# Optimization experiments

Hardware: AMD Instinct MI355X
Metric: run time of the kernel (lower is better)

Reference implementation:

```python
import jax, jax.numpy as jnp
import numpy as np

N, E, D, H = 50000, 800000, 128, 128
LN_EPS = 1e-3  # keras LayerNormalization default epsilon


def layer_norm(x, g, b):
    mu = jnp.mean(x, axis=-1, keepdims=True)
    var = jnp.mean(jnp.square(x - mu), axis=-1, keepdims=True)
    return (x - mu) * jax.lax.rsqrt(var + LN_EPS) * g + b


def mlp3(x, W1, b1, W2, b2, W3, b3, g1, be1, g2, be2):
    # 3-layer MLP: two hidden layers (relu + layernorm), linear output head
    h = layer_norm(jax.nn.relu(x @ W1 + b1), g1, be1)
    h = layer_norm(jax.nn.relu(h @ W2 + b2), g2, be2)
    return h @ W3 + b3


def _dense_init(key, fan_in, fan_out):
    return jax.random.normal(key, (fan_in, fan_out), jnp.float32) / np.sqrt(fan_in)


def setup_inputs() -> dict:
    key = jax.random.key(0)
    ks = jax.random.split(key, 12)
    query = jax.random.normal(ks[0], (N, D), jnp.float32)
    memory = jax.random.normal(ks[1], (N, D), jnp.float32)
    row = jnp.sort(jax.random.randint(ks[2], (E,), 0, N, jnp.int32))
    col = jax.random.randint(ks[3], (E,), 0, N, jnp.int32)
    # pre_process MLP: input 2D -> H -> H -> 1 (heads=1)
    pW1 = _dense_init(ks[4], 2 * D, H); pb1 = jnp.zeros((H,), jnp.float32)
    pW2 = _dense_init(ks[5], H, H);     pb2 = jnp.zeros((H,), jnp.float32)
    pW3 = _dense_init(ks[6], H, 1);     pb3 = jnp.zeros((1,), jnp.float32)
    pg1 = jnp.ones((H,), jnp.float32);  pbe1 = jnp.zeros((H,), jnp.float32)
    pg2 = jnp.ones((H,), jnp.float32);  pbe2 = jnp.zeros((H,), jnp.float32)
    # memory MLP: D -> H -> H -> H
    mW1 = _dense_init(ks[7], D, H); mb1 = jnp.zeros((H,), jnp.float32)
    mW2 = _dense_init(ks[8], H, H); mb2 = jnp.zeros((H,), jnp.float32)
    mW3 = _dense_init(ks[9], H, H); mb3 = jnp.zeros((H,), jnp.float32)
    mg1 = jnp.ones((H,), jnp.float32); mbe1 = jnp.zeros((H,), jnp.float32)
    mg2 = jnp.ones((H,), jnp.float32); mbe2 = jnp.zeros((H,), jnp.float32)
    return dict(query=query, memory=memory, row=row, col=col,
                pW1=pW1, pb1=pb1, pW2=pW2, pb2=pb2, pW3=pW3, pb3=pb3,
                pg1=pg1, pbe1=pbe1, pg2=pg2, pbe2=pbe2,
                mW1=mW1, mb1=mb1, mW2=mW2, mb2=mb2, mW3=mW3, mb3=mb3,
                mg1=mg1, mbe1=mbe1, mg2=mg2, mbe2=mbe2)


def reference(query, memory, row, col,
              pW1, pb1, pW2, pb2, pW3, pb3, pg1, pbe1, pg2, pbe2,
              mW1, mb1, mW2, mb2, mW3, mb3, mg1, mbe1, mg2, mbe2):
    # per-edge gather of query (target) and memory (source) node features
    units = jnp.concatenate([query[row], memory[col]], axis=-1)  # [E, 2D]
    h = jnp.tanh(mlp3(units, pW1, pb1, pW2, pb2, pW3, pb3, pg1, pbe1, pg2, pbe2))[:, 0]  # [E]
    mem_head = mlp3(memory, mW1, mb1, mW2, mb2, mW3, mb3, mg1, mbe1, mg2, mbe2)  # [N, H]
    # sparse_dense_matmul: out[i] = sum_{edges (i,j)} h_e * mem_head[j]
    out = jax.ops.segment_sum(h[:, None] * mem_head[col], row, num_segments=N)  # [N, H]
    return out
```

## Files before the change

### kernel.cpp

```cpp
#include <hip/hip_runtime.h>
#include <hip/hip_bf16.h>

typedef __attribute__((ext_vector_type(8))) short  svec8;
typedef __attribute__((ext_vector_type(4))) short  svec4;
typedef __attribute__((ext_vector_type(8))) __bf16 bfvec8;
typedef __attribute__((ext_vector_type(4))) float  f32x4;
typedef __attribute__((ext_vector_type(2))) float  f32x2;
typedef __attribute__((ext_vector_type(4))) unsigned uvec4;

#define LN_EPS 1e-3f

__device__ __forceinline__ short f2bf(float f) {
  union { float f; unsigned u; } v; v.f = f;
  unsigned u = v.u;
  u += 0x7fff + ((u >> 16) & 1);
  return (short)(u >> 16);
}

__device__ __forceinline__ unsigned pk2(float a, float b) {
  unsigned short ua = __builtin_bit_cast(unsigned short, (__bf16)a);
  unsigned short ub = __builtin_bit_cast(unsigned short, (__bf16)b);
  return (unsigned)ua | ((unsigned)ub << 16);
}

__device__ __forceinline__ f32x2 up2(unsigned w) {
  f32x2 r;
  r[0] = __builtin_bit_cast(float, w << 16);
  r[1] = __builtin_bit_cast(float, w & 0xffff0000u);
  return r;
}

__device__ __forceinline__ f32x4 mfma16(svec8 a, svec8 b, f32x4 c) {
  return __builtin_amdgcn_mfma_f32_16x16x32_bf16(
      __builtin_bit_cast(bfvec8, a), __builtin_bit_cast(bfvec8, b), c, 0, 0, 0);
}

__global__ __launch_bounds__(256) void setup_kernel(
    const float* __restrict__ pW1, const float* __restrict__ pW2,
    const float* __restrict__ pg1,
    const float* __restrict__ mW1, const float* __restrict__ mW2,
    const float* __restrict__ mW3,
    short* __restrict__ w1qp, short* __restrict__ w1mp,
    short* __restrict__ w2p,  short* __restrict__ mw1p,
    short* __restrict__ mw2p, short* __restrict__ mw3p,
    const int* __restrict__ row, int E, int N, int* __restrict__ off,
    const float* __restrict__ g1, const float* __restrict__ be1,
    const float* __restrict__ b2, const float* __restrict__ g2,
    const float* __restrict__ w3, const float* __restrict__ be2,
    const float* __restrict__ b3,
    float* __restrict__ s2, float* __restrict__ b2pv,
    float* __restrict__ gw, float* __restrict__ consts, int nboff)
{
  const int b = blockIdx.x;
  const int tid = threadIdx.x;
  if (b < 384) {
    int idx = b * 256 + tid;
    int which = idx >> 14, p = idx & 16383;
    int j = p & 7, lane = (p >> 3) & 63, t = p >> 9;
    int nf = t & 7, ks = t >> 3;
    int k = ks * 32 + (lane >> 4) * 8 + j;
    int n = nf * 16 + (lane & 15);
    const float* src; short* dst; float scale = 1.f;
    switch (which) {
      case 0:  src = pW1;         dst = w1qp; break;
      case 1:  src = pW1 + 16384; dst = w1mp; break;
      case 2:  src = pW2;         dst = w2p; scale = pg1[k]; break;
      case 3:  src = mW1;         dst = mw1p; break;
      case 4:  src = mW2;         dst = mw2p; break;
      default: src = mW3;         dst = mw3p; break;
    }
    dst[p] = f2bf(scale * src[k * 128 + n]);
  } else if (b < 384 + nboff) {
    int i = (b - 384) * 256 + tid;
    if (i > N) return;
    int lo = 0, hi = E;
    while (lo < hi) { int mid = (lo + hi) >> 1; if (row[mid] < i) lo = mid + 1; else hi = mid; }
    off[i] = lo;
  } else {
    __shared__ float tmp[256];
    int n = tid;
    if (n < 128) {
      float s = 0.f, bb = 0.f;
      for (int k = 0; k < 128; ++k) {
        float w = pW2[k * 128 + n];
        s  = fmaf(g1[k],  w, s);
        bb = fmaf(be1[k], w, bb);
      }
      s2[n]   = s;
      b2pv[n] = bb + b2[n];
      float g = g2[n] * w3[n];
      gw[n] = g;
      tmp[n]       = g;
      tmp[128 + n] = be2[n] * w3[n];
    }
    __syncthreads();
    if (n == 0) {
      float a = 0.f, c = 0.f;
      for (int i = 0; i < 128; ++i) { a += tmp[i]; c += tmp[128 + i]; }
      consts[0] = a;
      consts[1] = c + b3[0];
    }
  }
}

__global__ __launch_bounds__(256) void node_kernel(
    const float* __restrict__ mem, const float* __restrict__ query,
    const short* __restrict__ w1p, const short* __restrict__ w2p, const short* __restrict__ w3p,
    const short* __restrict__ wmp, const short* __restrict__ wqp,
    const float* __restrict__ b1v, const float* __restrict__ b2v, const float* __restrict__ b3v,
    const float* __restrict__ g1v, const float* __restrict__ be1v,
    const float* __restrict__ g2v, const float* __restrict__ be2v,
    const float* __restrict__ pb1,
    short* __restrict__ mhb, short* __restrict__ mwt, short* __restrict__ qwt,
    int N, int nbm)
{
  __shared__ short Xs[64 * 128];
  __shared__ short H1s[64 * 128];
  __shared__ float redA[4][64];
  __shared__ float redB[4][64];

  const int tid  = threadIdx.x;
  const int wv   = tid >> 6;
  const int lane = tid & 63;
  const int g16  = lane >> 4;
  const int l16  = lane & 15;
  const bool is_mem = (blockIdx.x < nbm);
  const int r0   = (is_mem ? blockIdx.x : blockIdx.x - nbm) * 64;
  const float* src = is_mem ? mem : query;

  #pragma unroll
  for (int it = 0; it < 8; ++it) {
    int c = tid + it * 256;
    int r = c >> 5;
    int part = c & 31;
    int gr = r0 + r; if (gr >= N) gr = N - 1;
    f32x4 v = *(const f32x4*)(src + (size_t)gr * 128 + part * 4);
    svec4 s;
    s[0] = f2bf(v[0]); s[1] = f2bf(v[1]); s[2] = f2bf(v[2]); s[3] = f2bf(v[3]);
    int b = (r * 256 + part * 8) ^ ((r & 7) << 4);
    *(svec4*)((char*)Xs + b) = s;
  }
  __syncthreads();

  const int nfb = wv * 2;
  const int col0 = wv * 32 + l16, col1 = col0 + 16;

  if (!is_mem) {
    f32x4 acc[4][2];
    #pragma unroll
    for (int mf = 0; mf < 4; ++mf) { f32x4 z = {0.f,0.f,0.f,0.f}; acc[mf][0] = z; acc[mf][1] = z; }
    #pragma unroll
    for (int ks = 0; ks < 4; ++ks) {
      svec8 bw0 = *(const svec8*)(wqp + (((ks * 8 + nfb + 0) * 64 + lane) << 3));
      svec8 bw1 = *(const svec8*)(wqp + (((ks * 8 + nfb + 1) * 64 + lane) << 3));
      #pragma unroll
      for (int mf = 0; mf < 4; ++mf) {
        int row = mf * 16 + l16;
        int byt = (row * 256 + ks * 64 + g16 * 16) ^ ((row & 7) << 4);
        svec8 a = *(const svec8*)((const char*)Xs + byt);
        acc[mf][0] = mfma16(a, bw0, acc[mf][0]);
        acc[mf][1] = mfma16(a, bw1, acc[mf][1]);
      }
    }
    float bi0 = pb1[col0], bi1 = pb1[col1];
    #pragma unroll
    for (int mf = 0; mf < 4; ++mf)
      #pragma unroll
      for (int r = 0; r < 4; ++r) {
        int rr = mf * 16 + g16 * 4 + r;
        int gr = r0 + rr;
        if (gr < N) {
          qwt[(size_t)gr * 128 + col0] = f2bf(acc[mf][0][r] + bi0);
          qwt[(size_t)gr * 128 + col1] = f2bf(acc[mf][1][r] + bi1);
        }
      }
    return;
  }

  f32x4 acc[4][2], accm[4][2];
  #pragma unroll
  for (int mf = 0; mf < 4; ++mf) {
    f32x4 z = {0.f,0.f,0.f,0.f};
    acc[mf][0] = z; acc[mf][1] = z; accm[mf][0] = z; accm[mf][1] = z;
  }
  #pragma unroll
  for (int ks = 0; ks < 4; ++ks) {
    svec8 bw0 = *(const svec8*)(w1p + (((ks * 8 + nfb + 0) * 64 + lane) << 3));
    svec8 bw1 = *(const svec8*)(w1p + (((ks * 8 + nfb + 1) * 64 + lane) << 3));
    svec8 bm0 = *(const svec8*)(wmp + (((ks * 8 + nfb + 0) * 64 + lane) << 3));
    svec8 bm1 = *(const svec8*)(wmp + (((ks * 8 + nfb + 1) * 64 + lane) << 3));
    #pragma unroll
    for (int mf = 0; mf < 4; ++mf) {
      int row = mf * 16 + l16;
      int byt = (row * 256 + ks * 64 + g16 * 16) ^ ((row & 7) << 4);
      svec8 a = *(const svec8*)((const char*)Xs + byt);
      acc[mf][0]  = mfma16(a, bw0, acc[mf][0]);
      acc[mf][1]  = mfma16(a, bw1, acc[mf][1]);
      accm[mf][0] = mfma16(a, bm0, accm[mf][0]);
      accm[mf][1] = mfma16(a, bm1, accm[mf][1]);
    }
  }
  #pragma unroll
  for (int mf = 0; mf < 4; ++mf)
    #pragma unroll
    for (int r = 0; r < 4; ++r) {
      int rr = mf * 16 + g16 * 4 + r;
      int gr = r0 + rr;
      if (gr < N) {
        mwt[(size_t)gr * 128 + col0] = f2bf(accm[mf][0][r]);
        mwt[(size_t)gr * 128 + col1] = f2bf(accm[mf][1][r]);
      }
    }

  float bi0 = b1v[col0], bi1 = b1v[col1];
  float ga0 = g1v[col0], ga1 = g1v[col1];
  float bb0 = be1v[col0], bb1 = be1v[col1];
  float y[4][2][4], ps[4][4], pq[4][4];
  #pragma unroll
  for (int mf = 0; mf < 4; ++mf)
    #pragma unroll
    for (int r = 0; r < 4; ++r) {
      float y0 = fmaxf(acc[mf][0][r] + bi0, 0.f);
      float y1 = fmaxf(acc[mf][1][r] + bi1, 0.f);
      y[mf][0][r] = y0; y[mf][1][r] = y1;
      ps[mf][r] = y0 + y1;
      pq[mf][r] = y0 * y0 + y1 * y1;
    }
  #pragma unroll
  for (int mk = 1; mk <= 8; mk <<= 1)
    #pragma unroll
    for (int mf = 0; mf < 4; ++mf)
      #pragma unroll
      for (int r = 0; r < 4; ++r) {
        ps[mf][r] += __shfl_xor(ps[mf][r], mk, 64);
        pq[mf][r] += __shfl_xor(pq[mf][r], mk, 64);
      }
  if (l16 == 0) {
    #pragma unroll
    for (int mf = 0; mf < 4; ++mf)
      #pragma unroll
      for (int r = 0; r < 4; ++r) {
        redA[wv][mf * 16 + g16 * 4 + r] = ps[mf][r];
        redB[wv][mf * 16 + g16 * 4 + r] = pq[mf][r];
      }
  }
  __syncthreads();
  #pragma unroll
  for (int mf = 0; mf < 4; ++mf)
    #pragma unroll
    for (int r = 0; r < 4; ++r) {
      int rr = mf * 16 + g16 * 4 + r;
      float s = redA[0][rr] + redA[1][rr] + redA[2][rr] + redA[3][rr];
      float q = redB[0][rr] + redB[1][rr] + redB[2][rr] + redB[3][rr];
      float mu = s * (1.f / 128.f);
      float var = fmaxf(q * (1.f / 128.f) - mu * mu, 0.f);
      float rstd = rsqrtf(var + LN_EPS);
      float z0 = (y[mf][0][r] - mu) * rstd * ga0 + bb0;
      float z1 = (y[mf][1][r] - mu) * rstd * ga1 + bb1;
      int by0 = (rr * 256 + col0 * 2) ^ ((rr & 7) << 4);
      int by1 = (rr * 256 + col1 * 2) ^ ((rr & 7) << 4);
      *(short*)((char*)H1s + by0) = f2bf(z0);
      *(short*)((char*)H1s + by1) = f2bf(z1);
    }
  __syncthreads();

  f32x4 acc2[4][2];
  #pragma unroll
  for (int mf = 0; mf < 4; ++mf) { f32x4 z = {0.f,0.f,0.f,0.f}; acc2[mf][0] = z; acc2[mf][1] = z; }
  #pragma unroll
  for (int ks = 0; ks < 4; ++ks) {
    svec8 bw0 = *(const svec8*)(w2p + (((ks * 8 + nfb + 0) * 64 + lane) << 3));
    svec8 bw1 = *(const svec8*)(w2p + (((ks * 8 + nfb + 1) * 64 + lane) << 3));
    #pragma unroll
    for (int mf = 0; mf < 4; ++mf) {
      int row = mf * 16 + l16;
      int byt = (row * 256 + ks * 64 + g16 * 16) ^ ((row & 7) << 4);
      svec8 a = *(const svec8*)((const char*)H1s + byt);
      acc2[mf][0] = mfma16(a, bw0, acc2[mf][0]);
      acc2[mf][1] = mfma16(a, bw1, acc2[mf][1]);
    }
  }

  float bi20 = b2v[col0], bi21 = b2v[col1];
  float ga20 = g2v[col0], ga21 = g2v[col1];
  float bb20 = be2v[col0], bb21 = be2v[col1];
  float y2[4][2][4];
  #pragma unroll
  for (int mf = 0; mf < 4; ++mf)
    #pragma unroll
    for (int r = 0; r < 4; ++r) {
      float y0 = fmaxf(acc2[mf][0][r] + bi20, 0.f);
      float y1 = fmaxf(acc2[mf][1][r] + bi21, 0.f);
      y2[mf][0][r] = y0; y2[mf][1][r] = y1;
      ps[mf][r] = y0 + y1;
      pq[mf][r] = y0 * y0 + y1 * y1;
    }
  #pragma unroll
  for (int mk = 1; mk <= 8; mk <<= 1)
    #pragma unroll
    for (int mf = 0; mf < 4; ++mf)
      #pragma unroll
      for (int r = 0; r < 4; ++r) {
        ps[mf][r] += __shfl_xor(ps[mf][r], mk, 64);
        pq[mf][r] += __shfl_xor(pq[mf][r], mk, 64);
      }
  if (l16 == 0) {
    #pragma unroll
    for (int mf = 0; mf < 4; ++mf)
      #pragma unroll
      for (int r = 0; r < 4; ++r) {
        redA[wv][mf * 16 + g16 * 4 + r] = ps[mf][r];
        redB[wv][mf * 16 + g16 * 4 + r] = pq[mf][r];
      }
  }
  __syncthreads();
  #pragma unroll
  for (int mf = 0; mf < 4; ++mf)
    #pragma unroll
    for (int r = 0; r < 4; ++r) {
      int rr = mf * 16 + g16 * 4 + r;
      float s = redA[0][rr] + redA[1][rr] + redA[2][rr] + redA[3][rr];
      float q = redB[0][rr] + redB[1][rr] + redB[2][rr] + redB[3][rr];
      float mu = s * (1.f / 128.f);
      float var = fmaxf(q * (1.f / 128.f) - mu * mu, 0.f);
      float rstd = rsqrtf(var + LN_EPS);
      float z0 = (y2[mf][0][r] - mu) * rstd * ga20 + bb20;
      float z1 = (y2[mf][1][r] - mu) * rstd * ga21 + bb21;
      int by0 = (rr * 256 + col0 * 2) ^ ((rr & 7) << 4);
      int by1 = (rr * 256 + col1 * 2) ^ ((rr & 7) << 4);
      *(short*)((char*)Xs + by0) = f2bf(z0);
      *(short*)((char*)Xs + by1) = f2bf(z1);
    }
  __syncthreads();

  f32x4 acc3[4][2];
  #pragma unroll
  for (int mf = 0; mf < 4; ++mf) { f32x4 z = {0.f,0.f,0.f,0.f}; acc3[mf][0] = z; acc3[mf][1] = z; }
  #pragma unroll
  for (int ks = 0; ks < 4; ++ks) {
    svec8 bw0 = *(const svec8*)(w3p + (((ks * 8 + nfb + 0) * 64 + lane) << 3));
    svec8 bw1 = *(const svec8*)(w3p + (((ks * 8 + nfb + 1) * 64 + lane) << 3));
    #pragma unroll
    for (int mf = 0; mf < 4; ++mf) {
      int row = mf * 16 + l16;
      int byt = (row * 256 + ks * 64 + g16 * 16) ^ ((row & 7) << 4);
      svec8 a = *(const svec8*)((const char*)Xs + byt);
      acc3[mf][0] = mfma16(a, bw0, acc3[mf][0]);
      acc3[mf][1] = mfma16(a, bw1, acc3[mf][1]);
    }
  }
  float bi30 = b3v[col0], bi31 = b3v[col1];
  #pragma unroll
  for (int mf = 0; mf < 4; ++mf)
    #pragma unroll
    for (int r = 0; r < 4; ++r) {
      int rr = mf * 16 + g16 * 4 + r;
      int gr = r0 + rr;
      if (gr < N) {
        mhb[(size_t)gr * 128 + col0] = f2bf(acc3[mf][0][r] + bi30);
        mhb[(size_t)gr * 128 + col1] = f2bf(acc3[mf][1][r] + bi31);
      }
    }
}

__device__ __forceinline__ void relu_stats(const svec8* qv, const svec8* mv,
                                           svec8* yf, float& ps_o, float& pq_o) {
  f32x2 psv = {0.f, 0.f}, pqv = {0.f, 0.f};
  #pragma unroll
  for (int ks2 = 0; ks2 < 4; ++ks2) {
    uvec4 qu = __builtin_bit_cast(uvec4, qv[ks2]);
    uvec4 mu = __builtin_bit_cast(uvec4, mv[ks2]);
    uvec4 u;
    #pragma unroll
    for (int p = 0; p < 4; ++p) {
      f32x2 y = __builtin_elementwise_max(up2(qu[p]) + up2(mu[p]), (f32x2){0.f, 0.f});
      psv += y;
      pqv += y * y;
      u[p] = pk2(y[0], y[1]);
    }
    yf[ks2] = __builtin_bit_cast(svec8, u);
  }
  float ps = psv[0] + psv[1], pq = pqv[0] + pqv[1];
  ps += __shfl_xor(ps, 16, 64); pq += __shfl_xor(pq, 16, 64);
  ps += __shfl_xor(ps, 32, 64); pq += __shfl_xor(pq, 32, 64);
  ps_o = ps; pq_o = pq;
}

__device__ __forceinline__ void epilogue(const f32x4* acc2, float rstd1, float mu1,
    const float* s2v, const float* b2pv, const float* gwv, float Sgw, float cb,
    float* __restrict__ hout, int e, bool valid, int lane, int g) {
  f32x2 rst = {rstd1, rstd1};
  f32x2 nmu = {-rstd1 * mu1, -rstd1 * mu1};
  f32x2 psv = {0.f,0.f}, pqv = {0.f,0.f}, pwv = {0.f,0.f};
  #pragma unroll
  for (int nf = 0; nf < 8; ++nf) {
    f32x4 s2 = *(const f32x4*)(s2v  + nf * 16 + g * 4);
    f32x4 bb = *(const f32x4*)(b2pv + nf * 16 + g * 4);
    f32x4 gw = *(const f32x4*)(gwv  + nf * 16 + g * 4);
    #pragma unroll
    for (int p = 0; p < 2; ++p) {
      f32x2 a   = { acc2[nf][2*p], acc2[nf][2*p+1] };
      f32x2 s2p = { s2[2*p], s2[2*p+1] };
      f32x2 bbp = { bb[2*p], bb[2*p+1] };
      f32x2 gwp = { gw[2*p], gw[2*p+1] };
      f32x2 h = rst * a + (nmu * s2p + bbp);
      f32x2 y = __builtin_elementwise_max(h, (f32x2){0.f, 0.f});
      psv += y;
      pqv += y * y;
      pwv += y * gwp;
    }
  }
  float ps2 = psv[0] + psv[1], pq2 = pqv[0] + pqv[1], pw2 = pwv[0] + pwv[1];
  ps2 += __shfl_xor(ps2, 16, 64); pq2 += __shfl_xor(pq2, 16, 64); pw2 += __shfl_xor(pw2, 16, 64);
  ps2 += __shfl_xor(ps2, 32, 64); pq2 += __shfl_xor(pq2, 32, 64); pw2 += __shfl_xor(pw2, 32, 64);
  float mu2   = ps2 * (1.f / 128.f);
  float var2  = fmaxf(pq2 * (1.f / 128.f) - mu2 * mu2, 0.f);
  float rstd2 = rsqrtf(var2 + LN_EPS);
  float p3 = fmaf(rstd2, pw2 - mu2 * Sgw, cb);
  if (lane < 16 && valid) hout[e] = tanhf(p3);
}

__global__ __launch_bounds__(256, 3) void edge_mlp_kernel(
    const short* __restrict__ qwt, const short* __restrict__ mwt,
    const int* __restrict__ rowi, const int* __restrict__ coli,
    const short* __restrict__ w2p,
    const float* __restrict__ s2v, const float* __restrict__ b2pv,
    const float* __restrict__ gwv, const float* __restrict__ consts,
    float* __restrict__ hout, int E)
{
  __shared__ short w2s[16384];

  const int tid  = threadIdx.x;
  const int wv   = tid >> 6;
  const int lane = tid & 63;
  const int g    = lane >> 4;
  const int l16  = lane & 15;

  const int nb  = gridDim.x;
  const int q8  = nb >> 3, r8 = nb & 7;
  const int xcd = blockIdx.x & 7, sub = blockIdx.x >> 3;
  const int bid = (xcd < r8 ? xcd * (q8 + 1) : r8 * (q8 + 1) + (xcd - r8) * q8) + sub;

  #pragma unroll
  for (int it = 0; it < 8; ++it) {
    int o = (it * 256 + tid) * 8;
    *(f32x4*)(w2s + o) = *(const f32x4*)(w2p + o);
  }
  __syncthreads();

  const int eb = bid * 128 + wv * 32;
  const int e0 = eb + l16, e1 = eb + 16 + l16;
  const bool v0 = (e0 < E), v1 = (e1 < E);
  const int ee0 = v0 ? e0 : 0, ee1 = v1 ? e1 : 0;
  const short* q0 = qwt + (size_t)rowi[ee0] * 128 + g * 8;
  const short* m0 = mwt + (size_t)coli[ee0] * 128 + g * 8;
  const short* q1 = qwt + (size_t)rowi[ee1] * 128 + g * 8;
  const short* m1 = mwt + (size_t)coli[ee1] * 128 + g * 8;

  svec8 qv0[4], mv0[4], qv1[4], mv1[4];
  #pragma unroll
  for (int ks2 = 0; ks2 < 4; ++ks2) {
    qv0[ks2] = *(const svec8*)(q0 + ks2 * 32);
    mv0[ks2] = *(const svec8*)(m0 + ks2 * 32);
    qv1[ks2] = *(const svec8*)(q1 + ks2 * 32);
    mv1[ks2] = *(const svec8*)(m1 + ks2 * 32);
  }

  svec8 yf0[4], yf1[4];
  float ps0, pq0, ps1, pq1;
  relu_stats(qv0, mv0, yf0, ps0, pq0);
  relu_stats(qv1, mv1, yf1, ps1, pq1);
  float mu1_0   = ps0 * (1.f / 128.f);
  float rstd1_0 = rsqrtf(fmaxf(pq0 * (1.f / 128.f) - mu1_0 * mu1_0, 0.f) + LN_EPS);
  float mu1_1   = ps1 * (1.f / 128.f);
  float rstd1_1 = rsqrtf(fmaxf(pq1 * (1.f / 128.f) - mu1_1 * mu1_1, 0.f) + LN_EPS);

  f32x4 acc2a[8], acc2b[8];
  #pragma unroll
  for (int nf = 0; nf < 8; ++nf) { f32x4 z = {0.f,0.f,0.f,0.f}; acc2a[nf] = z; acc2b[nf] = z; }
  #pragma unroll
  for (int ks2 = 0; ks2 < 4; ++ks2) {
    #pragma unroll
    for (int nf = 0; nf < 8; ++nf) {
      svec8 w = *(const svec8*)(w2s + (((ks2 * 8 + nf) * 64 + lane) << 3));
      acc2a[nf] = mfma16(w, yf0[ks2], acc2a[nf]);
      acc2b[nf] = mfma16(w, yf1[ks2], acc2b[nf]);
    }
  }

  float Sgw = consts[0], cb = consts[1];
  epilogue(acc2a, rstd1_0, mu1_0, s2v, b2pv, gwv, Sgw, cb, hout, e0, v0, lane, g);
  epilogue(acc2b, rstd1_1, mu1_1, s2v, b2pv, gwv, Sgw, cb, hout, e1, v1, lane, g);
}

__global__ __launch_bounds__(256) void segsum_kernel(
    const int* __restrict__ off, const int* __restrict__ coli,
    const float* __restrict__ hbuf, const short* __restrict__ mhb,
    float* __restrict__ out, int N)
{
  int wv = threadIdx.x >> 6, lane = threadIdx.x & 63;
  int i = blockIdx.x * 4 + wv;
  if (i >= N) return;
  int s = off[i], e = off[i + 1];
  f32x2 acc = {0.f, 0.f};
  int k = s;
  for (; k + 4 <= e; k += 4) {
    float h0 = hbuf[k], h1 = hbuf[k+1], h2 = hbuf[k+2], h3 = hbuf[k+3];
    unsigned w0 = *(const unsigned*)(mhb + (size_t)coli[k]   * 128 + lane * 2);
    unsigned w1 = *(const unsigned*)(mhb + (size_t)coli[k+1] * 128 + lane * 2);
    unsigned w2 = *(const unsigned*)(mhb + (size_t)coli[k+2] * 128 + lane * 2);
    unsigned w3 = *(const unsigned*)(mhb + (size_t)coli[k+3] * 128 + lane * 2);
    acc += (f32x2){h0, h0} * up2(w0);
    acc += (f32x2){h1, h1} * up2(w1);
    acc += (f32x2){h2, h2} * up2(w2);
    acc += (f32x2){h3, h3} * up2(w3);
  }
  for (; k < e; ++k) {
    float h = hbuf[k];
    unsigned w = *(const unsigned*)(mhb + (size_t)coli[k] * 128 + lane * 2);
    acc += (f32x2){h, h} * up2(w);
  }
  *(f32x2*)(out + (size_t)i * 128 + lane * 2) = acc;
}

extern "C" void kernel_launch(void* const* d_in, const int* in_sizes, int n_in,
                              void* d_out, int out_size, void* d_ws, size_t ws_size,
                              hipStream_t stream) {
  const float* query = (const float*)d_in[0];
  const float* mem   = (const float*)d_in[1];
  const int*   row   = (const int*)d_in[2];
  const int*   col   = (const int*)d_in[3];
  const float* pW1 = (const float*)d_in[4];  const float* pb1 = (const float*)d_in[5];
  const float* pW2 = (const float*)d_in[6];  const float* pb2 = (const float*)d_in[7];
  const float* pW3 = (const float*)d_in[8];  const float* pb3 = (const float*)d_in[9];
  const float* pg1 = (const float*)d_in[10]; const float* pbe1 = (const float*)d_in[11];
  const float* pg2 = (const float*)d_in[12]; const float* pbe2 = (const float*)d_in[13];
  const float* mW1 = (const float*)d_in[14]; const float* mb1 = (const float*)d_in[15];
  const float* mW2 = (const float*)d_in[16]; const float* mb2 = (const float*)d_in[17];
  const float* mW3 = (const float*)d_in[18]; const float* mb3 = (const float*)d_in[19];
  const float* mg1 = (const float*)d_in[20]; const float* mbe1 = (const float*)d_in[21];
  const float* mg2 = (const float*)d_in[22]; const float* mbe2 = (const float*)d_in[23];

  const int N = in_sizes[0] / 128;
  const int E = in_sizes[2];

  char* ws = (char*)d_ws;
  short* w1qp = (short*)(ws + 0);
  short* w1mp = (short*)(ws + 32768);
  short* w2p  = (short*)(ws + 65536);
  short* mw1p = (short*)(ws + 98304);
  short* mw2p = (short*)(ws + 131072);
  short* mw3p = (short*)(ws + 163840);
  float* s2v  = (float*)(ws + 196608);
  float* b2pv = (float*)(ws + 197120);
  float* gwv  = (float*)(ws + 197632);
  float* cons = (float*)(ws + 198144);
  int*   offs = (int*)(ws + 198208);
  size_t o = 198208 + (((size_t)(N + 1) * 4 + 255) / 256) * 256;
  short* qwt  = (short*)(ws + o);  o += (size_t)N * 128 * 2;
  short* mwt  = (short*)(ws + o);  o += (size_t)N * 128 * 2;
  short* mhb  = (short*)(ws + o);  o += (size_t)N * 128 * 2;
  float* hbuf = (float*)(ws + o);  o += (size_t)E * 4;

  if (ws_size < o) return;

  const int nboff = (N + 1 + 255) / 256;
  setup_kernel<<<384 + nboff + 1, 256, 0, stream>>>(
      pW1, pW2, pg1, mW1, mW2, mW3, w1qp, w1mp, w2p, mw1p, mw2p, mw3p,
      row, E, N, offs,
      pg1, pbe1, pb2, pg2, pW3, pbe2, pb3, s2v, b2pv, gwv, cons, nboff);

  const int nbm = (N + 63) / 64;
  node_kernel<<<2 * nbm, 256, 0, stream>>>(
      mem, query, mw1p, mw2p, mw3p, w1mp, w1qp,
      mb1, mb2, mb3, mg1, mbe1, mg2, mbe2, pb1,
      mhb, mwt, qwt, N, nbm);

  edge_mlp_kernel<<<(E + 127) / 128, 256, 0, stream>>>(
      qwt, mwt, row, col, w2p, s2v, b2pv, gwv, cons, hbuf, E);

  segsum_kernel<<<(N + 3) / 4, 256, 0, stream>>>(offs, col, hbuf, mhb, (float*)d_out, N);
}
```

Before: 180.9 us.

## Make edge MLP persistent with double-buffered gathers; unroll segsum by eight

The edge MLP kernel now launches a fixed grid of 512 blocks. Each block walks a contiguous range of 128-edge tiles and prefetches the next tile's gathered query/memory rows into a second register buffer while it processes the current one. This hides gather latency and loads the W2 weights into LDS once per block instead of once per tile. The cost is more registers, so occupancy drops from 3 to 2 blocks per CU. The segment-sum loop also unrolls from 4 to 8 edges to put more gather loads in flight.

```diff
diff --git a/kernel.cpp b/kernel.cpp
--- a/kernel.cpp
+++ b/kernel.cpp
@@ -420,13 +420,68 @@
   if (lane < 16 && valid) hout[e] = tanhf(p3);
 }
 
-__global__ __launch_bounds__(256, 3) void edge_mlp_kernel(
+struct EdgeBuf {
+  svec8 q0[4], m0[4], q1[4], m1[4];
+  int e0, e1;
+  bool v0, v1;
+};
+
+__device__ __forceinline__ void edge_load(EdgeBuf& B, int tile, int wv, int l16, int g,
+    const int* __restrict__ rowi, const int* __restrict__ coli,
+    const short* __restrict__ qwt, const short* __restrict__ mwt, int E) {
+  int eb = tile * 128 + wv * 32;
+  B.e0 = eb + l16; B.e1 = eb + 16 + l16;
+  B.v0 = (B.e0 < E); B.v1 = (B.e1 < E);
+  int ee0 = B.v0 ? B.e0 : 0, ee1 = B.v1 ? B.e1 : 0;
+  const short* q0 = qwt + (size_t)rowi[ee0] * 128 + g * 8;
+  const short* m0 = mwt + (size_t)coli[ee0] * 128 + g * 8;
+  const short* q1 = qwt + (size_t)rowi[ee1] * 128 + g * 8;
+  const short* m1 = mwt + (size_t)coli[ee1] * 128 + g * 8;
+  #pragma unroll
+  for (int ks2 = 0; ks2 < 4; ++ks2) {
+    B.q0[ks2] = *(const svec8*)(q0 + ks2 * 32);
+    B.m0[ks2] = *(const svec8*)(m0 + ks2 * 32);
+    B.q1[ks2] = *(const svec8*)(q1 + ks2 * 32);
+    B.m1[ks2] = *(const svec8*)(m1 + ks2 * 32);
+  }
+}
+
+__device__ __forceinline__ void edge_process(const EdgeBuf& B, const short* __restrict__ w2s,
+    const float* __restrict__ s2v, const float* __restrict__ b2pv,
+    const float* __restrict__ gwv, float Sgw, float cb,
+    float* __restrict__ hout, int lane, int g) {
+  svec8 yf0[4], yf1[4];
+  float ps0, pq0, ps1, pq1;
+  relu_stats(B.q0, B.m0, yf0, ps0, pq0);
+  relu_stats(B.q1, B.m1, yf1, ps1, pq1);
+  float mu1_0   = ps0 * (1.f / 128.f);
+  float rstd1_0 = rsqrtf(fmaxf(pq0 * (1.f / 128.f) - mu1_0 * mu1_0, 0.f) + LN_EPS);
+  float mu1_1   = ps1 * (1.f / 128.f);
+  float rstd1_1 = rsqrtf(fmaxf(pq1 * (1.f / 128.f) - mu1_1 * mu1_1, 0.f) + LN_EPS);
+
+  f32x4 acc2a[8], acc2b[8];
+  #pragma unroll
+  for (int nf = 0; nf < 8; ++nf) { f32x4 z = {0.f,0.f,0.f,0.f}; acc2a[nf] = z; acc2b[nf] = z; }
+  #pragma unroll
+  for (int ks2 = 0; ks2 < 4; ++ks2) {
+    #pragma unroll
+    for (int nf = 0; nf < 8; ++nf) {
+      svec8 w = *(const svec8*)(w2s + (((ks2 * 8 + nf) * 64 + lane) << 3));
+      acc2a[nf] = mfma16(w, yf0[ks2], acc2a[nf]);
+      acc2b[nf] = mfma16(w, yf1[ks2], acc2b[nf]);
+    }
+  }
+  epilogue(acc2a, rstd1_0, mu1_0, s2v, b2pv, gwv, Sgw, cb, hout, B.e0, B.v0, lane, g);
+  epilogue(acc2b, rstd1_1, mu1_1, s2v, b2pv, gwv, Sgw, cb, hout, B.e1, B.v1, lane, g);
+}
+
+__global__ __launch_bounds__(256, 2) void edge_mlp_kernel(
     const short* __restrict__ qwt, const short* __restrict__ mwt,
     const int* __restrict__ rowi, const int* __restrict__ coli,
     const short* __restrict__ w2p,
     const float* __restrict__ s2v, const float* __restrict__ b2pv,
     const float* __restrict__ gwv, const float* __restrict__ consts,
-    float* __restrict__ hout, int E)
+    float* __restrict__ hout, int E, int ntiles)
 {
   __shared__ short w2s[16384];
 
@@ -437,9 +492,9 @@
   const int l16  = lane & 15;
 
   const int nb  = gridDim.x;
-  const int q8  = nb >> 3, r8 = nb & 7;
-  const int xcd = blockIdx.x & 7, sub = blockIdx.x >> 3;
-  const int bid = (xcd < r8 ? xcd * (q8 + 1) : r8 * (q8 + 1) + (xcd - r8) * q8) + sub;
+  const int bid = (blockIdx.x & 7) * (nb >> 3) + (blockIdx.x >> 3);
+  const int t0  = (int)((long long)bid * ntiles / nb);
+  const int t1  = (int)((long long)(bid + 1) * ntiles / nb);
 
   #pragma unroll
   for (int it = 0; it < 8; ++it) {
@@ -448,49 +503,20 @@
   }
   __syncthreads();
 
-  const int eb = bid * 128 + wv * 32;
-  const int e0 = eb + l16, e1 = eb + 16 + l16;
-  const bool v0 = (e0 < E), v1 = (e1 < E);
-  const int ee0 = v0 ? e0 : 0, ee1 = v1 ? e1 : 0;
-  const short* q0 = qwt + (size_t)rowi[ee0] * 128 + g * 8;
-  const short* m0 = mwt + (size_t)coli[ee0] * 128 + g * 8;
-  const short* q1 = qwt + (size_t)rowi[ee1] * 128 + g * 8;
-  const short* m1 = mwt + (size_t)coli[ee1] * 128 + g * 8;
-
-  svec8 qv0[4], mv0[4], qv1[4], mv1[4];
-  #pragma unroll
-  for (int ks2 = 0; ks2 < 4; ++ks2) {
-    qv0[ks2] = *(const svec8*)(q0 + ks2 * 32);
-    mv0[ks2] = *(const svec8*)(m0 + ks2 * 32);
-    qv1[ks2] = *(const svec8*)(q1 + ks2 * 32);
-    mv1[ks2] = *(const svec8*)(m1 + ks2 * 32);
-  }
-
-  svec8 yf0[4], yf1[4];
-  float ps0, pq0, ps1, pq1;
-  relu_stats(qv0, mv0, yf0, ps0, pq0);
-  relu_stats(qv1, mv1, yf1, ps1, pq1);
-  float mu1_0   = ps0 * (1.f / 128.f);
-  float rstd1_0 = rsqrtf(fmaxf(pq0 * (1.f / 128.f) - mu1_0 * mu1_0, 0.f) + LN_EPS);
-  float mu1_1   = ps1 * (1.f / 128.f);
-  float rstd1_1 = rsqrtf(fmaxf(pq1 * (1.f / 128.f) - mu1_1 * mu1_1, 0.f) + LN_EPS);
-
-  f32x4 acc2a[8], acc2b[8];
-  #pragma unroll
-  for (int nf = 0; nf < 8; ++nf) { f32x4 z = {0.f,0.f,0.f,0.f}; acc2a[nf] = z; acc2b[nf] = z; }
-  #pragma unroll
-  for (int ks2 = 0; ks2 < 4; ++ks2) {
-    #pragma unroll
-    for (int nf = 0; nf < 8; ++nf) {
-      svec8 w = *(const svec8*)(w2s + (((ks2 * 8 + nf) * 64 + lane) << 3));
-      acc2a[nf] = mfma16(w, yf0[ks2], acc2a[nf]);
-      acc2b[nf] = mfma16(w, yf1[ks2], acc2b[nf]);
-    }
-  }
-
-  float Sgw = consts[0], cb = consts[1];
-  epilogue(acc2a, rstd1_0, mu1_0, s2v, b2pv, gwv, Sgw, cb, hout, e0, v0, lane, g);
-  epilogue(acc2b, rstd1_1, mu1_1, s2v, b2pv, gwv, Sgw, cb, hout, e1, v1, lane, g);
+  const float Sgw = consts[0], cb = consts[1];
+
+  EdgeBuf A, B;
+  int t = t0;
+  if (t < t1) edge_load(A, t, wv, l16, g, rowi, coli, qwt, mwt, E);
+  while (t < t1) {
+    if (t + 1 < t1) edge_load(B, t + 1, wv, l16, g, rowi, coli, qwt, mwt, E);
+    edge_process(A, w2s, s2v, b2pv, gwv, Sgw, cb, hout, lane, g);
+    ++t;
+    if (t >= t1) break;
+    if (t + 1 < t1) edge_load(A, t + 1, wv, l16, g, rowi, coli, qwt, mwt, E);
+    edge_process(B, w2s, s2v, b2pv, gwv, Sgw, cb, hout, lane, g);
+    ++t;
+  }
 }
 
 __global__ __launch_bounds__(256) void segsum_kernel(
@@ -504,16 +530,16 @@
   int s = off[i], e = off[i + 1];
   f32x2 acc = {0.f, 0.f};
   int k = s;
-  for (; k + 4 <= e; k += 4) {
-    float h0 = hbuf[k], h1 = hbuf[k+1], h2 = hbuf[k+2], h3 = hbuf[k+3];
-    unsigned w0 = *(const unsigned*)(mhb + (size_t)coli[k]   * 128 + lane * 2);
-    unsigned w1 = *(const unsigned*)(mhb + (size_t)coli[k+1] * 128 + lane * 2);
-    unsigned w2 = *(const unsigned*)(mhb + (size_t)coli[k+2] * 128 + lane * 2);
-    unsigned w3 = *(const unsigned*)(mhb + (size_t)coli[k+3] * 128 + lane * 2);
-    acc += (f32x2){h0, h0} * up2(w0);
-    acc += (f32x2){h1, h1} * up2(w1);
-    acc += (f32x2){h2, h2} * up2(w2);
-    acc += (f32x2){h3, h3} * up2(w3);
+  for (; k + 8 <= e; k += 8) {
+    float h[8]; unsigned w[8];
+    #pragma unroll
+    for (int u = 0; u < 8; ++u) {
+      h[u] = hbuf[k + u];
+      w[u] = *(const unsigned*)(mhb + (size_t)coli[k + u] * 128 + lane * 2);
+    }
+    #pragma unroll
+    for (int u = 0; u < 8; ++u)
+      acc += (f32x2){h[u], h[u]} * up2(w[u]);
   }
   for (; k < e; ++k) {
     float h = hbuf[k];
@@ -576,8 +602,9 @@
       mb1, mb2, mb3, mg1, mbe1, mg2, mbe2, pb1,
       mhb, mwt, qwt, N, nbm);
 
-  edge_mlp_kernel<<<(E + 127) / 128, 256, 0, stream>>>(
-      qwt, mwt, row, col, w2p, s2v, b2pv, gwv, cons, hbuf, E);
+  const int ntiles = (E + 127) / 128;
+  edge_mlp_kernel<<<512, 256, 0, stream>>>(
+      qwt, mwt, row, col, w2p, s2v, b2pv, gwv, cons, hbuf, E, ntiles);
 
   segsum_kernel<<<(N + 3) / 4, 256, 0, stream>>>(offs, col, hbuf, mhb, (float*)d_out, N);
 }
```

New measurement: 404.6 us. 2.24x slower.
